# Optimization experiments

Measured on AMD Instinct MI355X. Metric: run time of the kernel, lower is better.

The kernel has to match this reference:

```python
import jax, jax.numpy as jnp
import numpy as np
from jax import lax

START_IDX = 0
END_IDX = 1
NEG = -10000.0


def setup_inputs() -> dict:
    key = jax.random.key(0)
    k_h, k_t = jax.random.split(key)
    seq_len, tagset_size = 8192, 2048
    h = jax.random.normal(k_h, (seq_len, tagset_size), dtype=jnp.float32)
    transitions = jax.random.normal(k_t, (tagset_size, tagset_size), dtype=jnp.float32)
    # CRF constraints: nothing transitions FROM end into start row; nothing transitions TO end col
    transitions = transitions.at[START_IDX, :].set(NEG)
    transitions = transitions.at[:, END_IDX].set(NEG)
    return {"h": h, "transitions": transitions}


def reference(h, transitions):
    # h: [S, T] emission scores; transitions: [T, T], transitions[i, j] = score(j -> i)
    T = transitions.shape[0]
    init = jnp.full((T,), NEG, dtype=h.dtype).at[START_IDX].set(0.0)

    def step(forward_var, emit):
        # scores[i, j] = forward_var[j] + transitions[i, j] + emit[i]
        scores = forward_var[None, :] + transitions + emit[:, None]  # [T, T]
        return jax.nn.logsumexp(scores, axis=-1), None

    forward_var, _ = lax.scan(step, init, h)
    terminal = forward_var + transitions[END_IDX]
    return jax.nn.logsumexp(terminal)
```

## Files before the change

kernel.cpp:

```cpp
#include <hip/hip_runtime.h>


#define TSZ   2048
#define NCH   32
#define NW    8
#define CH_LEN 256
#define BURN  24
#define TCYC  (CH_LEN + BURN)
#define START_I 0
#define END_I   1

typedef float v4f __attribute__((ext_vector_type(4)));
typedef _Float16 h2f __attribute__((ext_vector_type(2)));

__device__ __forceinline__ h2f pk16(float a, float b) {
    return __builtin_bit_cast(h2f, __builtin_amdgcn_cvt_pkrtz(a, b));
}
__device__ __forceinline__ void st_coh(float* p, float v) {
    asm volatile("global_store_dword %0, %1, off sc0 sc1"
                 :: "v"(p), "v"(v) : "memory");
}
__device__ __forceinline__ float ld_coh1(const float* p) {
    float r;
    asm volatile("global_load_dword %0, %1, off sc0 sc1\n\ts_waitcnt vmcnt(0)"
                 : "=&v"(r) : "v"(p) : "memory");
    return r;
}
__device__ __forceinline__ v4f ld_coh4(const float* p) {
    v4f r;
    asm volatile("global_load_dwordx4 %0, %1, off sc0 sc1\n\ts_waitcnt vmcnt(0)"
                 : "=&v"(r) : "v"(p) : "memory");
    return r;
}

__global__ __launch_bounds__(512, 1)
void crf_chain(const float* __restrict__ h, const float* __restrict__ tr,
               float* __restrict__ out, float* __restrict__ ws)
{
    const int tid  = threadIdx.x;
    const int lane = tid & 63;
    const int wv   = tid >> 6;
    const int blk  = blockIdx.x;
    const int g    = blk >> 4;
    const int b    = blk & 15;
    const int ca   = g;
    const int cb   = g + 16;
    const int row_base = b * 128 + wv * 16;

    float* u_bufs = ws;
    float* usave  = ws + NCH * 2 * TSZ;
    float* ufin   = usave + NCH * TSZ;
    float* cbuf   = ufin + NCH * TSZ;
    int*   posts  = (int*)((char*)ws + 1048704);

    __shared__ unsigned long long els64[32][512];
    __shared__ unsigned long long uh_sh[2][512];

    h2f e2r[12][16];
    #pragma unroll
    for (int r = 0; r < 12; ++r) {
        const float* trow = tr + (size_t)(row_base + r) * TSZ + 4 * lane;
        #pragma unroll
        for (int k = 0; k < 8; ++k) {
            float4 t4 = *(const float4*)(trow + 256 * k);
            e2r[r][2 * k]     = pk16(__expf(t4.x), __expf(t4.y));
            e2r[r][2 * k + 1] = pk16(__expf(t4.z), __expf(t4.w));
        }
    }
    #pragma unroll
    for (int rr = 0; rr < 4; ++rr) {
        const float* trow = tr + (size_t)(row_base + 12 + rr) * TSZ + 4 * lane;
        #pragma unroll
        for (int k = 0; k < 8; ++k) {
            float4 t4 = *(const float4*)(trow + 256 * k);
            unsigned lo = __builtin_bit_cast(unsigned, pk16(__expf(t4.x), __expf(t4.y)));
            unsigned hi = __builtin_bit_cast(unsigned, pk16(__expf(t4.z), __expf(t4.w)));
            els64[wv * 4 + rr][lane + 64 * k] =
                ((unsigned long long)hi << 32) | (unsigned long long)lo;
        }
    }

    const int q    = ((lane & 1) << 2) | (lane & 2) | ((lane >> 2) & 1);
    const int grow = row_base + q;

    const int skX = ca * CH_LEN, seX = skX + CH_LEN;
    const int s0X = (ca == 0) ? 0 : (skX - BURN);
    const int TX  = (ca == 0) ? CH_LEN : TCYC;
    const int skY = cb * CH_LEN, seY = skY + CH_LEN;
    const int s0Y = skY - BURN;

    float* ubX = u_bufs + ca * 2 * TSZ;
    float* ubY = u_bufs + cb * 2 * TSZ;

    if (tid < 128) {
        int row = b * 128 + tid;
        st_coh(&ubX[row], (ca == 0) ? ((row == START_I) ? 1.0f : 0.0f) : 1.0f);
        st_coh(&ubY[row], 1.0f);
    }

    float ChatX = 0.0f, ChatY = 0.0f;

    auto POLL_PACK = [&](const float* ubase, int par, int in_neg, int cslot,
                         bool kept, float& ch) {
        const float* pa = ubase + par * TSZ + 4 * lane;
        const float* pb = pa + 1024;
        v4f u0, u1, u2, u3, u4, u5, u6, u7;
        for (;;) {
            asm volatile(
                "global_load_dwordx4 %0, %8, off sc0 sc1\n\t"
                "global_load_dwordx4 %1, %8, off offset:1024 sc0 sc1\n\t"
                "global_load_dwordx4 %2, %8, off offset:2048 sc0 sc1\n\t"
                "global_load_dwordx4 %3, %8, off offset:3072 sc0 sc1\n\t"
                "global_load_dwordx4 %4, %9, off sc0 sc1\n\t"
                "global_load_dwordx4 %5, %9, off offset:1024 sc0 sc1\n\t"
                "global_load_dwordx4 %6, %9, off offset:2048 sc0 sc1\n\t"
                "global_load_dwordx4 %7, %9, off offset:3072 sc0 sc1\n\t"
                "s_waitcnt vmcnt(0)"
                : "=&v"(u0), "=&v"(u1), "=&v"(u2), "=&v"(u3),
                  "=&v"(u4), "=&v"(u5), "=&v"(u6), "=&v"(u7)
                : "v"(pa), "v"(pb)
                : "memory");
            bool fresh;
            if (in_neg) {
                int a = __float_as_int(u0.x) & __float_as_int(u0.y) & __float_as_int(u0.z) & __float_as_int(u0.w);
                a &= __float_as_int(u1.x) & __float_as_int(u1.y) & __float_as_int(u1.z) & __float_as_int(u1.w);
                a &= __float_as_int(u2.x) & __float_as_int(u2.y) & __float_as_int(u2.z) & __float_as_int(u2.w);
                a &= __float_as_int(u3.x) & __float_as_int(u3.y) & __float_as_int(u3.z) & __float_as_int(u3.w);
                a &= __float_as_int(u4.x) & __float_as_int(u4.y) & __float_as_int(u4.z) & __float_as_int(u4.w);
                a &= __float_as_int(u5.x) & __float_as_int(u5.y) & __float_as_int(u5.z) & __float_as_int(u5.w);
                a &= __float_as_int(u6.x) & __float_as_int(u6.y) & __float_as_int(u6.z) & __float_as_int(u6.w);
                a &= __float_as_int(u7.x) & __float_as_int(u7.y) & __float_as_int(u7.z) & __float_as_int(u7.w);
                fresh = (a < 0);
            } else {
                int o = __float_as_int(u0.x) | __float_as_int(u0.y) | __float_as_int(u0.z) | __float_as_int(u0.w);
                o |= __float_as_int(u1.x) | __float_as_int(u1.y) | __float_as_int(u1.z) | __float_as_int(u1.w);
                o |= __float_as_int(u2.x) | __float_as_int(u2.y) | __float_as_int(u2.z) | __float_as_int(u2.w);
                o |= __float_as_int(u3.x) | __float_as_int(u3.y) | __float_as_int(u3.z) | __float_as_int(u3.w);
                o |= __float_as_int(u4.x) | __float_as_int(u4.y) | __float_as_int(u4.z) | __float_as_int(u4.w);
                o |= __float_as_int(u5.x) | __float_as_int(u5.y) | __float_as_int(u5.z) | __float_as_int(u5.w);
                o |= __float_as_int(u6.x) | __float_as_int(u6.y) | __float_as_int(u6.z) | __float_as_int(u6.w);
                o |= __float_as_int(u7.x) | __float_as_int(u7.y) | __float_as_int(u7.z) | __float_as_int(u7.w);
                fresh = (o >= 0);
            }
            if (__all(fresh)) break;
        }
        float m;
        m =          fmaxf(fmaxf(fabsf(u0.x), fabsf(u0.y)), fmaxf(fabsf(u0.z), fabsf(u0.w)));
        m = fmaxf(m, fmaxf(fmaxf(fabsf(u1.x), fabsf(u1.y)), fmaxf(fabsf(u1.z), fabsf(u1.w))));
        m = fmaxf(m, fmaxf(fmaxf(fabsf(u2.x), fabsf(u2.y)), fmaxf(fabsf(u2.z), fabsf(u2.w))));
        m = fmaxf(m, fmaxf(fmaxf(fabsf(u3.x), fabsf(u3.y)), fmaxf(fabsf(u3.z), fabsf(u3.w))));
        m = fmaxf(m, fmaxf(fmaxf(fabsf(u4.x), fabsf(u4.y)), fmaxf(fabsf(u4.z), fabsf(u4.w))));
        m = fmaxf(m, fmaxf(fmaxf(fabsf(u5.x), fabsf(u5.y)), fmaxf(fabsf(u5.z), fabsf(u5.w))));
        m = fmaxf(m, fmaxf(fmaxf(fabsf(u6.x), fabsf(u6.y)), fmaxf(fabsf(u6.z), fabsf(u6.w))));
        m = fmaxf(m, fmaxf(fmaxf(fabsf(u7.x), fabsf(u7.y)), fmaxf(fabsf(u7.z), fabsf(u7.w))));
        #pragma unroll
        for (int d = 1; d < 64; d <<= 1) m = fmaxf(m, __shfl_xor(m, d, 64));

        const float rn = (in_neg ? -1.0f : 1.0f) / m;
        v4f mine = (wv < 4) ? ((wv < 2) ? ((wv == 0) ? u0 : u1)
                                        : ((wv == 2) ? u2 : u3))
                            : ((wv < 6) ? ((wv == 4) ? u4 : u5)
                                        : ((wv == 6) ? u6 : u7));
        unsigned lo = __builtin_bit_cast(unsigned, pk16(mine.x * rn, mine.y * rn));
        unsigned hi = __builtin_bit_cast(unsigned, pk16(mine.z * rn, mine.w * rn));
        uh_sh[cslot][lane + 64 * wv] =
            ((unsigned long long)hi << 32) | (unsigned long long)lo;
        if (kept) ch += __logf(m);
    };

    auto GEMV_COMPUTE = [&](const unsigned long long* uh_src, float& outA, float& outB) {
        h2f uh[16];
        #pragma unroll
        for (int k = 0; k < 8; ++k) {
            unsigned long long qw = uh_src[lane + 64 * k];
            uh[2 * k]     = __builtin_bit_cast(h2f, (unsigned)qw);
            uh[2 * k + 1] = __builtin_bit_cast(h2f, (unsigned)(qw >> 32));
        }
        float acc[8];
        #pragma unroll
        for (int r = 0; r < 8; ++r) acc[r] = 0.0f;
        #pragma unroll
        for (int k = 0; k < 16; ++k) {
            #pragma unroll
            for (int r = 0; r < 8; ++r)
                acc[r] = __builtin_amdgcn_fdot2(e2r[r][k], uh[k], acc[r], false);
        }
        #pragma unroll
        for (int r = 0; r < 4; ++r) {
            float send = (lane & 1) ? acc[r] : acc[r + 4];
            float recv = __shfl_xor(send, 1, 64);
            float keep = (lane & 1) ? acc[r + 4] : acc[r];
            acc[r] = keep + recv;
        }
        #pragma unroll
        for (int r = 0; r < 2; ++r) {
            float send = (lane & 2) ? acc[r] : acc[r + 2];
            float recv = __shfl_xor(send, 2, 64);
            float keep = (lane & 2) ? acc[r + 2] : acc[r];
            acc[r] = keep + recv;
        }
        {
            float send = (lane & 4) ? acc[0] : acc[1];
            float recv = __shfl_xor(send, 4, 64);
            float keep = (lane & 4) ? acc[1] : acc[0];
            acc[0] = keep + recv;
        }
        acc[0] += __shfl_xor(acc[0], 8, 64);
        acc[0] += __shfl_xor(acc[0], 16, 64);
        acc[0] += __shfl_xor(acc[0], 32, 64);
        outA = acc[0];

        #pragma unroll
        for (int r = 0; r < 8; ++r) acc[r] = 0.0f;
        #pragma unroll
        for (int k = 0; k < 8; ++k) {
            unsigned long long q0 = els64[wv * 4 + 0][lane + 64 * k];
            unsigned long long q1 = els64[wv * 4 + 1][lane + 64 * k];
            unsigned long long q2 = els64[wv * 4 + 2][lane + 64 * k];
            unsigned long long q3 = els64[wv * 4 + 3][lane + 64 * k];
            #pragma unroll
            for (int r = 0; r < 4; ++r) {
                acc[r] = __builtin_amdgcn_fdot2(e2r[8 + r][2 * k],     uh[2 * k],     acc[r], false);
                acc[r] = __builtin_amdgcn_fdot2(e2r[8 + r][2 * k + 1], uh[2 * k + 1], acc[r], false);
            }
            acc[4] = __builtin_amdgcn_fdot2(__builtin_bit_cast(h2f, (unsigned)q0),         uh[2 * k],     acc[4], false);
            acc[4] = __builtin_amdgcn_fdot2(__builtin_bit_cast(h2f, (unsigned)(q0 >> 32)), uh[2 * k + 1], acc[4], false);
            acc[5] = __builtin_amdgcn_fdot2(__builtin_bit_cast(h2f, (unsigned)q1),         uh[2 * k],     acc[5], false);
            acc[5] = __builtin_amdgcn_fdot2(__builtin_bit_cast(h2f, (unsigned)(q1 >> 32)), uh[2 * k + 1], acc[5], false);
            acc[6] = __builtin_amdgcn_fdot2(__builtin_bit_cast(h2f, (unsigned)q2),         uh[2 * k],     acc[6], false);
            acc[6] = __builtin_amdgcn_fdot2(__builtin_bit_cast(h2f, (unsigned)(q2 >> 32)), uh[2 * k + 1], acc[6], false);
            acc[7] = __builtin_amdgcn_fdot2(__builtin_bit_cast(h2f, (unsigned)q3),         uh[2 * k],     acc[7], false);
            acc[7] = __builtin_amdgcn_fdot2(__builtin_bit_cast(h2f, (unsigned)(q3 >> 32)), uh[2 * k + 1], acc[7], false);
        }
        #pragma unroll
        for (int r = 0; r < 4; ++r) {
            float send = (lane & 1) ? acc[r] : acc[r + 4];
            float recv = __shfl_xor(send, 1, 64);
            float keep = (lane & 1) ? acc[r + 4] : acc[r];
            acc[r] = keep + recv;
        }
        #pragma unroll
        for (int r = 0; r < 2; ++r) {
            float send = (lane & 2) ? acc[r] : acc[r + 2];
            float recv = __shfl_xor(send, 2, 64);
            float keep = (lane & 2) ? acc[r + 2] : acc[r];
            acc[r] = keep + recv;
        }
        {
            float send = (lane & 4) ? acc[0] : acc[1];
            float recv = __shfl_xor(send, 4, 64);
            float keep = (lane & 4) ? acc[1] : acc[0];
            acc[0] = keep + recv;
        }
        acc[0] += __shfl_xor(acc[0], 8, 64);
        acc[0] += __shfl_xor(acc[0], 16, 64);
        acc[0] += __shfl_xor(acc[0], 32, 64);
        outB = acc[0];
    };

    auto BAR = [&]() {
        __builtin_amdgcn_sched_barrier(0);
        asm volatile("s_waitcnt lgkmcnt(0)" ::: "memory");
        __builtin_amdgcn_s_barrier();
        __builtin_amdgcn_sched_barrier(0);
    };

    POLL_PACK(ubX, 0, 0, 0, (s0X + 1) > skX, ChatX);
    BAR();

    for (int T = 0; T < TCYC; ++T) {
        const int outp = (T + 1) & 1, outn = ((T + 1) >> 1) & 1;

        {
            const int sX = s0X + T;
            const bool doX = (T < TX);
            float h0 = 0.0f, h1 = 0.0f;
            if (doX && lane < 8) {
                h0 = h[(size_t)sX * TSZ + grow];
                h1 = h[(size_t)sX * TSZ + grow + 8];
            }
            if (doX) {
                float rA, rB;
                GEMV_COMPUTE(&uh_sh[0][0], rA, rB);
                if (lane < 8) {
                    float utA = rA * __expf(h0);
                    float utB = rB * __expf(h1);
                    float* uo = ubX + outp * TSZ;
                    st_coh(&uo[grow],     outn ? -utA : utA);
                    st_coh(&uo[grow + 8], outn ? -utB : utB);
                    if (ca > 0 && sX + 1 == skX) {
                        st_coh(&usave[ca * TSZ + grow],     utA);
                        st_coh(&usave[ca * TSZ + grow + 8], utB);
                    }
                    if (sX + 1 == seX) {
                        st_coh(&ufin[ca * TSZ + grow],     utA);
                        st_coh(&ufin[ca * TSZ + grow + 8], utB);
                    }
                }
            }
            POLL_PACK(ubY, T & 1, (T >> 1) & 1, 1, (s0Y + T + 1) > skY, ChatY);
            BAR();
        }

        {
            const int sY = s0Y + T;
            float h0 = 0.0f, h1 = 0.0f;
            if (lane < 8) {
                h0 = h[(size_t)sY * TSZ + grow];
                h1 = h[(size_t)sY * TSZ + grow + 8];
            }
            {
                float rA, rB;
                GEMV_COMPUTE(&uh_sh[1][0], rA, rB);
                if (lane < 8) {
                    float utA = rA * __expf(h0);
                    float utB = rB * __expf(h1);
                    float* uo = ubY + outp * TSZ;
                    st_coh(&uo[grow],     outn ? -utA : utA);
                    st_coh(&uo[grow + 8], outn ? -utB : utB);
                    if (sY + 1 == skY) {
                        st_coh(&usave[cb * TSZ + grow],     utA);
                        st_coh(&usave[cb * TSZ + grow + 8], utB);
                    }
                    if (sY + 1 == seY) {
                        st_coh(&ufin[cb * TSZ + grow],     utA);
                        st_coh(&ufin[cb * TSZ + grow + 8], utB);
                    }
                }
            }
            const int v = T + 1;
            if (v < TX)
                POLL_PACK(ubX, v & 1, (v >> 1) & 1, 0, (s0X + v + 1) > skX, ChatX);
            BAR();
        }
    }

    if (b == 0 && wv == 0 && lane == 0) {
        st_coh(&cbuf[ca], ChatX);
        st_coh(&cbuf[cb], ChatY);
    }
    asm volatile("s_waitcnt vmcnt(0)" ::: "memory");
    if (lane == 0)
        __hip_atomic_store(&posts[blk * NW + wv], 1,
                           __ATOMIC_RELAXED, __HIP_MEMORY_SCOPE_AGENT);

    if (blk == 0 && wv == 0) {
        int ok;
        do {
            __builtin_amdgcn_s_sleep(1);
            ok = 1;
            #pragma unroll
            for (int i = 0; i < 32; ++i) {
                int v = __hip_atomic_load(&posts[lane + 64 * i],
                                          __ATOMIC_RELAXED, __HIP_MEMORY_SCOPE_AGENT);
                ok &= (v == 1);
            }
        } while (!__all(ok));

        float O = 0.0f;
        for (int cc = 1; cc < NCH; ++cc) {
            float sa = 0.0f, sb = 0.0f;
            for (int j = 4 * lane; j < TSZ; j += 256) {
                v4f a4 = ld_coh4(&ufin[(cc - 1) * TSZ + j]);
                v4f b4 = ld_coh4(&usave[cc * TSZ + j]);
                sa += a4.x + a4.y + a4.z + a4.w;
                sb += b4.x + b4.y + b4.z + b4.w;
            }
            #pragma unroll
            for (int d = 1; d < 64; d <<= 1) {
                sa += __shfl_xor(sa, d, 64);
                sb += __shfl_xor(sb, d, 64);
            }
            O += ld_coh1(&cbuf[cc - 1]) + __logf(sa) - __logf(sb);
        }
        float se = 0.0f;
        for (int j = 4 * lane; j < TSZ; j += 256) {
            const float4 t4 = *(const float4*)(tr + (size_t)END_I * TSZ + j);
            v4f uf = ld_coh4(&ufin[(NCH - 1) * TSZ + j]);
            se += __expf(t4.x) * uf.x + __expf(t4.y) * uf.y +
                  __expf(t4.z) * uf.z + __expf(t4.w) * uf.w;
        }
        #pragma unroll
        for (int d = 1; d < 64; d <<= 1) se += __shfl_xor(se, d, 64);

        float ans = O + ld_coh1(&cbuf[NCH - 1]) + __logf(se);
        if (lane == 0) out[0] = ans;
    }
}

extern "C" void kernel_launch(void* const* d_in, const int* in_sizes, int n_in,
                              void* d_out, int out_size, void* d_ws, size_t ws_size,
                              hipStream_t stream) {
    const float* h  = (const float*)d_in[0];
    const float* tr = (const float*)d_in[1];
    (void)in_sizes; (void)n_in; (void)out_size; (void)ws_size;
    crf_chain<<<dim3(256), dim3(512), 0, stream>>>(h, tr, (float*)d_out, (float*)d_ws);
}
```

Before: 2.237 ms.

## Exchange fp16-packed state vectors with sign-tag polling, drop LDS staging and barriers

```diff
diff --git a/kernel.cpp b/kernel.cpp
--- a/kernel.cpp
+++ b/kernel.cpp
@@ -9,14 +9,20 @@
 #define TCYC  (CH_LEN + BURN)
 #define START_I 0
 #define END_I   1
+#define KAPPA 0.00390625f
 
 typedef float v4f __attribute__((ext_vector_type(4)));
+typedef unsigned v4u __attribute__((ext_vector_type(4)));
 typedef _Float16 h2f __attribute__((ext_vector_type(2)));
 
 __device__ __forceinline__ h2f pk16(float a, float b) {
     return __builtin_bit_cast(h2f, __builtin_amdgcn_cvt_pkrtz(a, b));
 }
 __device__ __forceinline__ void st_coh(float* p, float v) {
+    asm volatile("global_store_dword %0, %1, off sc0 sc1"
+                 :: "v"(p), "v"(v) : "memory");
+}
+__device__ __forceinline__ void st_cohu(unsigned* p, unsigned v) {
     asm volatile("global_store_dword %0, %1, off sc0 sc1"
                  :: "v"(p), "v"(v) : "memory");
 }
@@ -32,6 +38,45 @@
                  : "=&v"(r) : "v"(p) : "memory");
     return r;
 }
+
+#define ISSUE4(R0,R1,R2,R3,P)                                                 \
+    asm volatile(                                                             \
+        "global_load_dwordx4 %0, %4, off sc0 sc1\n\t"                         \
+        "global_load_dwordx4 %1, %4, off offset:1024 sc0 sc1\n\t"             \
+        "global_load_dwordx4 %2, %4, off offset:2048 sc0 sc1\n\t"             \
+        "global_load_dwordx4 %3, %4, off offset:3072 sc0 sc1"                 \
+        : "=&v"(R0), "=&v"(R1), "=&v"(R2), "=&v"(R3)                          \
+        : "v"(P) : "memory")
+
+#define RELOAD4(R0,R1,R2,R3,P)                                                \
+    asm volatile(                                                             \
+        "global_load_dwordx4 %0, %4, off sc0 sc1\n\t"                         \
+        "global_load_dwordx4 %1, %4, off offset:1024 sc0 sc1\n\t"             \
+        "global_load_dwordx4 %2, %4, off offset:2048 sc0 sc1\n\t"             \
+        "global_load_dwordx4 %3, %4, off offset:3072 sc0 sc1\n\t"             \
+        "s_waitcnt vmcnt(0)"                                                  \
+        : "=&v"(R0), "=&v"(R1), "=&v"(R2), "=&v"(R3)                          \
+        : "v"(P) : "memory")
+
+#define WAITFRESH(R0,R1,R2,R3,P,INNEG)                                        \
+    do {                                                                      \
+        asm volatile("s_waitcnt vmcnt(0)"                                     \
+                     : "+v"(R0), "+v"(R1), "+v"(R2), "+v"(R3) :: "memory");   \
+        for (;;) {                                                            \
+            unsigned am_ = 0xffffffffu, om_ = 0u;                             \
+            _Pragma("unroll")                                                 \
+            for (int d_ = 0; d_ < 4; ++d_) {                                  \
+                unsigned t_;                                                  \
+                t_ = R0[d_] & 0x80008000u; am_ &= t_; om_ |= t_;              \
+                t_ = R1[d_] & 0x80008000u; am_ &= t_; om_ |= t_;              \
+                t_ = R2[d_] & 0x80008000u; am_ &= t_; om_ |= t_;              \
+                t_ = R3[d_] & 0x80008000u; am_ &= t_; om_ |= t_;              \
+            }                                                                 \
+            bool fr_ = (INNEG) ? (am_ == 0x80008000u) : (om_ == 0u);          \
+            if (__all(fr_)) break;                                            \
+            RELOAD4(R0, R1, R2, R3, P);                                       \
+        }                                                                     \
+    } while (0)
 
 __global__ __launch_bounds__(512, 1)
 void crf_chain(const float* __restrict__ h, const float* __restrict__ tr,
@@ -47,34 +92,38 @@
     const int cb   = g + 16;
     const int row_base = b * 128 + wv * 16;
 
-    float* u_bufs = ws;
-    float* usave  = ws + NCH * 2 * TSZ;
-    float* ufin   = usave + NCH * TSZ;
-    float* cbuf   = ufin + NCH * TSZ;
-    int*   posts  = (int*)((char*)ws + 1048704);
+    unsigned* ub   = (unsigned*)ws;
+    float* wsf     = (float*)ws;
+    float* usave   = wsf + 65536;
+    float* ufin    = usave + NCH * TSZ;
+    float* cbuf    = ufin + NCH * TSZ;
+    int*   posts   = (int*)(wsf + 196672);
 
     __shared__ unsigned long long els64[32][512];
-    __shared__ unsigned long long uh_sh[2][512];
 
     h2f e2r[12][16];
     #pragma unroll
     for (int r = 0; r < 12; ++r) {
-        const float* trow = tr + (size_t)(row_base + r) * TSZ + 4 * lane;
-        #pragma unroll
-        for (int k = 0; k < 8; ++k) {
-            float4 t4 = *(const float4*)(trow + 256 * k);
-            e2r[r][2 * k]     = pk16(__expf(t4.x), __expf(t4.y));
-            e2r[r][2 * k + 1] = pk16(__expf(t4.z), __expf(t4.w));
+        const float* trow = tr + (size_t)(row_base + r) * TSZ;
+        #pragma unroll
+        for (int j = 0; j < 16; ++j) {
+            int D = 4 * lane + 256 * (j >> 2) + (j & 3);
+            int c = 16 * (D >> 3) + (D & 7);
+            e2r[r][j] = pk16(__expf(trow[c]), __expf(trow[c + 8]));
         }
     }
     #pragma unroll
     for (int rr = 0; rr < 4; ++rr) {
-        const float* trow = tr + (size_t)(row_base + 12 + rr) * TSZ + 4 * lane;
+        const float* trow = tr + (size_t)(row_base + 12 + rr) * TSZ;
         #pragma unroll
         for (int k = 0; k < 8; ++k) {
-            float4 t4 = *(const float4*)(trow + 256 * k);
-            unsigned lo = __builtin_bit_cast(unsigned, pk16(__expf(t4.x), __expf(t4.y)));
-            unsigned hi = __builtin_bit_cast(unsigned, pk16(__expf(t4.z), __expf(t4.w)));
+            int j0 = 2 * k, j1 = 2 * k + 1;
+            int D0 = 4 * lane + 256 * (j0 >> 2) + (j0 & 3);
+            int D1 = 4 * lane + 256 * (j1 >> 2) + (j1 & 3);
+            int c0 = 16 * (D0 >> 3) + (D0 & 7);
+            int c1 = 16 * (D1 >> 3) + (D1 & 7);
+            unsigned lo = __builtin_bit_cast(unsigned, pk16(__expf(trow[c0]), __expf(trow[c0 + 8])));
+            unsigned hi = __builtin_bit_cast(unsigned, pk16(__expf(trow[c1]), __expf(trow[c1 + 8])));
             els64[wv * 4 + rr][lane + 64 * k] =
                 ((unsigned long long)hi << 32) | (unsigned long long)lo;
         }
@@ -89,92 +138,47 @@
     const int skY = cb * CH_LEN, seY = skY + CH_LEN;
     const int s0Y = skY - BURN;
 
-    float* ubX = u_bufs + ca * 2 * TSZ;
-    float* ubY = u_bufs + cb * 2 * TSZ;
-
-    if (tid < 128) {
-        int row = b * 128 + tid;
-        st_coh(&ubX[row], (ca == 0) ? ((row == START_I) ? 1.0f : 0.0f) : 1.0f);
-        st_coh(&ubY[row], 1.0f);
-    }
+    unsigned* ubX = ub + ca * 2 * 1024;
+    unsigned* ubY = ub + cb * 2 * 1024;
+
+    for (int j = tid; j < 1024; j += 512) {
+        int rlo = 16 * (j >> 3) + (j & 7), rhi = rlo + 8;
+        float xa = (ca == 0) ? ((rlo == START_I) ? KAPPA : 0.0f) : KAPPA;
+        float xb = (ca == 0) ? ((rhi == START_I) ? KAPPA : 0.0f) : KAPPA;
+        st_cohu(&ubX[j], __builtin_bit_cast(unsigned, pk16(xa, xb)));
+        st_cohu(&ubY[j], __builtin_bit_cast(unsigned, pk16(KAPPA, KAPPA)));
+    }
+    __syncthreads();
 
     float ChatX = 0.0f, ChatY = 0.0f;
 
-    auto POLL_PACK = [&](const float* ubase, int par, int in_neg, int cslot,
-                         bool kept, float& ch) {
-        const float* pa = ubase + par * TSZ + 4 * lane;
-        const float* pb = pa + 1024;
-        v4f u0, u1, u2, u3, u4, u5, u6, u7;
-        for (;;) {
-            asm volatile(
-                "global_load_dwordx4 %0, %8, off sc0 sc1\n\t"
-                "global_load_dwordx4 %1, %8, off offset:1024 sc0 sc1\n\t"
-                "global_load_dwordx4 %2, %8, off offset:2048 sc0 sc1\n\t"
-                "global_load_dwordx4 %3, %8, off offset:3072 sc0 sc1\n\t"
-                "global_load_dwordx4 %4, %9, off sc0 sc1\n\t"
-                "global_load_dwordx4 %5, %9, off offset:1024 sc0 sc1\n\t"
-                "global_load_dwordx4 %6, %9, off offset:2048 sc0 sc1\n\t"
-                "global_load_dwordx4 %7, %9, off offset:3072 sc0 sc1\n\t"
-                "s_waitcnt vmcnt(0)"
-                : "=&v"(u0), "=&v"(u1), "=&v"(u2), "=&v"(u3),
-                  "=&v"(u4), "=&v"(u5), "=&v"(u6), "=&v"(u7)
-                : "v"(pa), "v"(pb)
-                : "memory");
-            bool fresh;
-            if (in_neg) {
-                int a = __float_as_int(u0.x) & __float_as_int(u0.y) & __float_as_int(u0.z) & __float_as_int(u0.w);
-                a &= __float_as_int(u1.x) & __float_as_int(u1.y) & __float_as_int(u1.z) & __float_as_int(u1.w);
-                a &= __float_as_int(u2.x) & __float_as_int(u2.y) & __float_as_int(u2.z) & __float_as_int(u2.w);
-                a &= __float_as_int(u3.x) & __float_as_int(u3.y) & __float_as_int(u3.z) & __float_as_int(u3.w);
-                a &= __float_as_int(u4.x) & __float_as_int(u4.y) & __float_as_int(u4.z) & __float_as_int(u4.w);
-                a &= __float_as_int(u5.x) & __float_as_int(u5.y) & __float_as_int(u5.z) & __float_as_int(u5.w);
-                a &= __float_as_int(u6.x) & __float_as_int(u6.y) & __float_as_int(u6.z) & __float_as_int(u6.w);
-                a &= __float_as_int(u7.x) & __float_as_int(u7.y) & __float_as_int(u7.z) & __float_as_int(u7.w);
-                fresh = (a < 0);
-            } else {
-                int o = __float_as_int(u0.x) | __float_as_int(u0.y) | __float_as_int(u0.z) | __float_as_int(u0.w);
-                o |= __float_as_int(u1.x) | __float_as_int(u1.y) | __float_as_int(u1.z) | __float_as_int(u1.w);
-                o |= __float_as_int(u2.x) | __float_as_int(u2.y) | __float_as_int(u2.z) | __float_as_int(u2.w);
-                o |= __float_as_int(u3.x) | __float_as_int(u3.y) | __float_as_int(u3.z) | __float_as_int(u3.w);
-                o |= __float_as_int(u4.x) | __float_as_int(u4.y) | __float_as_int(u4.z) | __float_as_int(u4.w);
-                o |= __float_as_int(u5.x) | __float_as_int(u5.y) | __float_as_int(u5.z) | __float_as_int(u5.w);
-                o |= __float_as_int(u6.x) | __float_as_int(u6.y) | __float_as_int(u6.z) | __float_as_int(u6.w);
-                o |= __float_as_int(u7.x) | __float_as_int(u7.y) | __float_as_int(u7.z) | __float_as_int(u7.w);
-                fresh = (o >= 0);
-            }
-            if (__all(fresh)) break;
-        }
-        float m;
-        m =          fmaxf(fmaxf(fabsf(u0.x), fabsf(u0.y)), fmaxf(fabsf(u0.z), fabsf(u0.w)));
-        m = fmaxf(m, fmaxf(fmaxf(fabsf(u1.x), fabsf(u1.y)), fmaxf(fabsf(u1.z), fabsf(u1.w))));
-        m = fmaxf(m, fmaxf(fmaxf(fabsf(u2.x), fabsf(u2.y)), fmaxf(fabsf(u2.z), fabsf(u2.w))));
-        m = fmaxf(m, fmaxf(fmaxf(fabsf(u3.x), fabsf(u3.y)), fmaxf(fabsf(u3.z), fabsf(u3.w))));
-        m = fmaxf(m, fmaxf(fmaxf(fabsf(u4.x), fabsf(u4.y)), fmaxf(fabsf(u4.z), fabsf(u4.w))));
-        m = fmaxf(m, fmaxf(fmaxf(fabsf(u5.x), fabsf(u5.y)), fmaxf(fabsf(u5.z), fabsf(u5.w))));
-        m = fmaxf(m, fmaxf(fmaxf(fabsf(u6.x), fabsf(u6.y)), fmaxf(fabsf(u6.z), fabsf(u6.w))));
-        m = fmaxf(m, fmaxf(fmaxf(fabsf(u7.x), fabsf(u7.y)), fmaxf(fabsf(u7.z), fabsf(u7.w))));
-        #pragma unroll
-        for (int d = 1; d < 64; d <<= 1) m = fmaxf(m, __shfl_xor(m, d, 64));
-
-        const float rn = (in_neg ? -1.0f : 1.0f) / m;
-        v4f mine = (wv < 4) ? ((wv < 2) ? ((wv == 0) ? u0 : u1)
-                                        : ((wv == 2) ? u2 : u3))
-                            : ((wv < 6) ? ((wv == 4) ? u4 : u5)
-                                        : ((wv == 6) ? u6 : u7));
-        unsigned lo = __builtin_bit_cast(unsigned, pk16(mine.x * rn, mine.y * rn));
-        unsigned hi = __builtin_bit_cast(unsigned, pk16(mine.z * rn, mine.w * rn));
-        uh_sh[cslot][lane + 64 * wv] =
-            ((unsigned long long)hi << 32) | (unsigned long long)lo;
-        if (kept) ch += __logf(m);
+    auto MAXRED = [&](v4u a0, v4u a1, v4u a2, v4u a3) -> float {
+        unsigned mm = 0;
+        #pragma unroll
+        for (int d = 0; d < 4; ++d) {
+            unsigned a;
+            a = a0[d] & 0x7fff7fffu; mm = mm > (a & 0xffffu) ? mm : (a & 0xffffu); mm = mm > (a >> 16) ? mm : (a >> 16);
+            a = a1[d] & 0x7fff7fffu; mm = mm > (a & 0xffffu) ? mm : (a & 0xffffu); mm = mm > (a >> 16) ? mm : (a >> 16);
+            a = a2[d] & 0x7fff7fffu; mm = mm > (a & 0xffffu) ? mm : (a & 0xffffu); mm = mm > (a >> 16) ? mm : (a >> 16);
+            a = a3[d] & 0x7fff7fffu; mm = mm > (a & 0xffffu) ? mm : (a & 0xffffu); mm = mm > (a >> 16) ? mm : (a >> 16);
+        }
+        #pragma unroll
+        for (int d = 1; d < 64; d <<= 1) {
+            unsigned o = (unsigned)__shfl_xor((int)mm, d, 64);
+            mm = mm > o ? mm : o;
+        }
+        _Float16 hf = __builtin_bit_cast(_Float16, (unsigned short)mm);
+        return (float)hf;
     };
 
-    auto GEMV_COMPUTE = [&](const unsigned long long* uh_src, float& outA, float& outB) {
+    auto GEMV = [&](v4u a0, v4u a1, v4u a2, v4u a3, float& oA, float& oB) {
         h2f uh[16];
         #pragma unroll
-        for (int k = 0; k < 8; ++k) {
-            unsigned long long qw = uh_src[lane + 64 * k];
-            uh[2 * k]     = __builtin_bit_cast(h2f, (unsigned)qw);
-            uh[2 * k + 1] = __builtin_bit_cast(h2f, (unsigned)(qw >> 32));
+        for (int d = 0; d < 4; ++d) {
+            uh[d]      = __builtin_bit_cast(h2f, a0[d]);
+            uh[4 + d]  = __builtin_bit_cast(h2f, a1[d]);
+            uh[8 + d]  = __builtin_bit_cast(h2f, a2[d]);
+            uh[12 + d] = __builtin_bit_cast(h2f, a3[d]);
         }
         float acc[8];
         #pragma unroll
@@ -208,7 +212,7 @@
         acc[0] += __shfl_xor(acc[0], 8, 64);
         acc[0] += __shfl_xor(acc[0], 16, 64);
         acc[0] += __shfl_xor(acc[0], 32, 64);
-        outA = acc[0];
+        oA = acc[0];
 
         #pragma unroll
         for (int r = 0; r < 8; ++r) acc[r] = 0.0f;
@@ -255,51 +259,57 @@
         acc[0] += __shfl_xor(acc[0], 8, 64);
         acc[0] += __shfl_xor(acc[0], 16, 64);
         acc[0] += __shfl_xor(acc[0], 32, 64);
-        outB = acc[0];
+        oB = acc[0];
     };
 
-    auto BAR = [&]() {
-        __builtin_amdgcn_sched_barrier(0);
-        asm volatile("s_waitcnt lgkmcnt(0)" ::: "memory");
-        __builtin_amdgcn_s_barrier();
-        __builtin_amdgcn_sched_barrier(0);
-    };
-
-    POLL_PACK(ubX, 0, 0, 0, (s0X + 1) > skX, ChatX);
-    BAR();
+    const int outD = 64 * b + 8 * wv + q;
+
+    v4u x0, x1, x2, x3, y0, y1, y2, y3;
+    const unsigned* pX0 = ubX + 4 * lane;
+    const unsigned* pX1 = ubX + 1024 + 4 * lane;
+    const unsigned* pY0 = ubY + 4 * lane;
+    const unsigned* pY1 = ubY + 1024 + 4 * lane;
+
+    ISSUE4(x0, x1, x2, x3, pX0);
 
     for (int T = 0; T < TCYC; ++T) {
         const int outp = (T + 1) & 1, outn = ((T + 1) >> 1) & 1;
-
-        {
+        const int inn  = (T >> 1) & 1;
+        const unsigned tagbits = outn ? 0x80008000u : 0u;
+        const unsigned* pXin = (T & 1) ? pX1 : pX0;
+        const unsigned* pYin = (T & 1) ? pY1 : pY0;
+
+        const bool doX = (T < TX);
+        if (doX) {
             const int sX = s0X + T;
-            const bool doX = (T < TX);
             float h0 = 0.0f, h1 = 0.0f;
-            if (doX && lane < 8) {
+            if (lane < 8) {
                 h0 = h[(size_t)sX * TSZ + grow];
                 h1 = h[(size_t)sX * TSZ + grow + 8];
             }
-            if (doX) {
-                float rA, rB;
-                GEMV_COMPUTE(&uh_sh[0][0], rA, rB);
-                if (lane < 8) {
-                    float utA = rA * __expf(h0);
-                    float utB = rB * __expf(h1);
-                    float* uo = ubX + outp * TSZ;
-                    st_coh(&uo[grow],     outn ? -utA : utA);
-                    st_coh(&uo[grow + 8], outn ? -utB : utB);
-                    if (ca > 0 && sX + 1 == skX) {
-                        st_coh(&usave[ca * TSZ + grow],     utA);
-                        st_coh(&usave[ca * TSZ + grow + 8], utB);
-                    }
-                    if (sX + 1 == seX) {
-                        st_coh(&ufin[ca * TSZ + grow],     utA);
-                        st_coh(&ufin[ca * TSZ + grow + 8], utB);
-                    }
+            WAITFRESH(x0, x1, x2, x3, pXin, inn);
+            ISSUE4(y0, y1, y2, y3, pYin);
+            float mX = MAXRED(x0, x1, x2, x3);
+            float rA, rB;
+            GEMV(x0, x1, x2, x3, rA, rB);
+            if (lane < 8) {
+                float invm = 1.0f / mX;
+                float PA = fabsf(rA) * __expf(h0) * invm;
+                float PB = fabsf(rB) * __expf(h1) * invm;
+                unsigned w = __builtin_bit_cast(unsigned, pk16(PA * KAPPA, PB * KAPPA)) | tagbits;
+                st_cohu(&ubX[outp * 1024 + outD], w);
+                if (ca > 0 && sX + 1 == skX) {
+                    st_coh(&usave[ca * TSZ + grow],     PA);
+                    st_coh(&usave[ca * TSZ + grow + 8], PB);
                 }
-            }
-            POLL_PACK(ubY, T & 1, (T >> 1) & 1, 1, (s0Y + T + 1) > skY, ChatY);
-            BAR();
+                if (sX + 1 == seX) {
+                    st_coh(&ufin[ca * TSZ + grow],     PA);
+                    st_coh(&ufin[ca * TSZ + grow + 8], PB);
+                }
+            }
+            if (sX + 1 > skX) ChatX += __logf(mX * 256.0f);
+        } else {
+            ISSUE4(y0, y1, y2, y3, pYin);
         }
 
         {
@@ -309,29 +319,30 @@
                 h0 = h[(size_t)sY * TSZ + grow];
                 h1 = h[(size_t)sY * TSZ + grow + 8];
             }
-            {
-                float rA, rB;
-                GEMV_COMPUTE(&uh_sh[1][0], rA, rB);
-                if (lane < 8) {
-                    float utA = rA * __expf(h0);
-                    float utB = rB * __expf(h1);
-                    float* uo = ubY + outp * TSZ;
-                    st_coh(&uo[grow],     outn ? -utA : utA);
-                    st_coh(&uo[grow + 8], outn ? -utB : utB);
-                    if (sY + 1 == skY) {
-                        st_coh(&usave[cb * TSZ + grow],     utA);
-                        st_coh(&usave[cb * TSZ + grow + 8], utB);
-                    }
-                    if (sY + 1 == seY) {
-                        st_coh(&ufin[cb * TSZ + grow],     utA);
-                        st_coh(&ufin[cb * TSZ + grow + 8], utB);
-                    }
+            WAITFRESH(y0, y1, y2, y3, pYin, inn);
+            if (T + 1 < TX) {
+                const unsigned* pXn = ((T + 1) & 1) ? pX1 : pX0;
+                ISSUE4(x0, x1, x2, x3, pXn);
+            }
+            float mY = MAXRED(y0, y1, y2, y3);
+            float rA, rB;
+            GEMV(y0, y1, y2, y3, rA, rB);
+            if (lane < 8) {
+                float invm = 1.0f / mY;
+                float PA = fabsf(rA) * __expf(h0) * invm;
+                float PB = fabsf(rB) * __expf(h1) * invm;
+                unsigned w = __builtin_bit_cast(unsigned, pk16(PA * KAPPA, PB * KAPPA)) | tagbits;
+                st_cohu(&ubY[outp * 1024 + outD], w);
+                if (sY + 1 == skY) {
+                    st_coh(&usave[cb * TSZ + grow],     PA);
+                    st_coh(&usave[cb * TSZ + grow + 8], PB);
                 }
-            }
-            const int v = T + 1;
-            if (v < TX)
-                POLL_PACK(ubX, v & 1, (v >> 1) & 1, 0, (s0X + v + 1) > skX, ChatX);
-            BAR();
+                if (sY + 1 == seY) {
+                    st_coh(&ufin[cb * TSZ + grow],     PA);
+                    st_coh(&ufin[cb * TSZ + grow + 8], PB);
+                }
+            }
+            if (sY + 1 > skY) ChatY += __logf(mY * 256.0f);
         }
     }
 
```

Result: slower. 2.332 ms (+4.2%).
